# Kernel optimization log

Measured on AMD Instinct MI355X. Metric: run time of the kernel, lower is better.

Reference implementation:

```python
import jax, jax.numpy as jnp
import numpy as np

VOCAB = 100000
D = 128
B = 256
L = 2048  # leaves per tree (power of two -> complete binary tree)


def setup_inputs() -> dict:
    key = jax.random.key(0)
    k1, k2, k3, k4 = jax.random.split(key, 4)
    word_ids = jax.random.randint(k1, (B, L), 0, VOCAB)
    embedding = jax.random.normal(k2, (VOCAB, D), dtype=jnp.float32) * 0.1
    # torch nn.Linear(2*D, D): weight [D, 2*D], bias [D]
    W = jax.random.normal(k3, (D, 2 * D), dtype=jnp.float32) * (1.0 / np.sqrt(2 * D))
    b = jax.random.normal(k4, (D,), dtype=jnp.float32) * 0.01
    return {"word_ids": word_ids, "embedding": embedding, "W": W, "b": b}


def reference(word_ids, embedding, W, b):
    # Leaves: embedding lookup for every leaf of every tree. [B, L, D]
    x = embedding[word_ids]
    # Internal nodes, batched by depth: each level combines adjacent pairs
    # via linear(concat(left, right)). log2(L) levels (static unroll).
    while x.shape[1] > 1:
        left = x[:, 0::2, :]   # [B, n/2, D]
        right = x[:, 1::2, :]  # [B, n/2, D]
        pair = jnp.concatenate([left, right], axis=-1)  # [B, n/2, 2D]
        x = jnp.einsum('bnd,od->bno', pair, W) + b      # [B, n/2, D]
    return x[:, 0, :]  # root result per tree, [B, D]
```

## Files before the change

kernel.cpp:

```cpp
#include <hip/hip_runtime.h>


typedef __bf16 bf16x8 __attribute__((ext_vector_type(8)));
typedef __bf16 bf16x4 __attribute__((ext_vector_type(4)));
typedef float f32x4 __attribute__((ext_vector_type(4)));

#define STRIDE 136

__global__ void pack_w_kernel(const float* __restrict__ W,
                              __bf16* __restrict__ wpack) {
    const int f = blockIdx.x;
    const int tid = threadIdx.x;
    const int wv = tid >> 6, l = tid & 63;
    const int nl = f >> 3, kk = f & 7;
    const int o = ((wv << 1) + nl) * 16 + (l & 15);
    const int d = kk * 32 + ((l >> 4) << 3);
    const float* src = W + o * 256 + d;
    bf16x8 h;
#pragma unroll
    for (int j = 0; j < 8; ++j) h[j] = (__bf16)src[j];
    *(bf16x8*)(wpack + (size_t)(f * 256 + tid) * 8) = h;
}

template <int NOUT>
__device__ __forceinline__ void level_step(
    const __bf16* src0, const __bf16* src1, __bf16* dst,
    const bf16x8* wf, const float* bval, int wv, int q, int lm)
{
    const int ntm = (NOUT + 15) >> 4;
#pragma unroll
    for (int mt = 0; mt < ntm; ++mt) {
        const __bf16* src = mt ? src1 : src0;
        const int me = (NOUT >= 16) ? lm : (lm < NOUT ? lm : 0);
        f32x4 acc[2];
        acc[0] = f32x4{ bval[0], bval[0], bval[0], bval[0] };
        acc[1] = f32x4{ bval[1], bval[1], bval[1], bval[1] };
#pragma unroll
        for (int kh = 0; kh < 2; ++kh) {
            const int row = 2 * me + kh;
            bf16x8 af[4];
#pragma unroll
            for (int j = 0; j < 4; ++j)
                af[j] = *(const bf16x8*)&src[row * STRIDE + j * 32 + q * 8];
#pragma unroll
            for (int nl = 0; nl < 2; ++nl)
#pragma unroll
                for (int j = 0; j < 4; ++j)
                    acc[nl] = __builtin_amdgcn_mfma_f32_16x16x32_bf16(
                        af[j], wf[nl * 8 + kh * 4 + j], acc[nl], 0, 0, 0);
        }
#pragma unroll
        for (int nl = 0; nl < 2; ++nl) {
            const int col = (2 * wv + nl) * 16 + lm;
            const bf16x4 hv = __builtin_convertvector(acc[nl], bf16x4);
#pragma unroll
            for (int r = 0; r < 4; ++r) {
                const int row = mt * 16 + q * 4 + r;
                if (row < NOUT)
                    dst[row * STRIDE + col] = hv[r];
            }
        }
    }
    __syncthreads();
}

__device__ __forceinline__ void level_final(
    const __bf16* src, __bf16* yrow,
    const bf16x8* wf, const float* bval, int wv, int q, int lm)
{
    const int me = (lm < 2) ? lm : 0;
    f32x4 acc[2];
    acc[0] = f32x4{ bval[0], bval[0], bval[0], bval[0] };
    acc[1] = f32x4{ bval[1], bval[1], bval[1], bval[1] };
#pragma unroll
    for (int kh = 0; kh < 2; ++kh) {
        const int row = 2 * me + kh;
        bf16x8 af[4];
#pragma unroll
        for (int j = 0; j < 4; ++j)
            af[j] = *(const bf16x8*)&src[row * STRIDE + j * 32 + q * 8];
#pragma unroll
        for (int nl = 0; nl < 2; ++nl)
#pragma unroll
            for (int j = 0; j < 4; ++j)
                acc[nl] = __builtin_amdgcn_mfma_f32_16x16x32_bf16(
                    af[j], wf[nl * 8 + kh * 4 + j], acc[nl], 0, 0, 0);
    }
#pragma unroll
    for (int nl = 0; nl < 2; ++nl) {
        const int col = (2 * wv + nl) * 16 + lm;
        if (q == 0) {
            yrow[0 * 128 + col] = (__bf16)acc[nl][0];
            yrow[1 * 128 + col] = (__bf16)acc[nl][1];
        }
    }
}

__device__ __forceinline__ void gather64(
    const int* wb64, const float* emb, __bf16* dstA, int tid)
{
    int idreg[8];
#pragma unroll
    for (int i = 0; i < 8; ++i) idreg[i] = wb64[(tid >> 5) + 8 * i];
#pragma unroll
    for (int i = 0; i < 8; ++i) {
        const int row = (tid >> 5) + 8 * i;
        const int c4 = tid & 31;
        const f32x4 v = *(const f32x4*)(emb + (size_t)idreg[i] * 128 + c4 * 4);
        *(bf16x4*)&dstA[row * STRIDE + c4 * 4] =
            __builtin_convertvector(v, bf16x4);
    }
}

__global__ __launch_bounds__(256, 4) void tree128_kernel(
    const int* __restrict__ wid, const float* __restrict__ emb,
    const __bf16* __restrict__ wpack, const float* __restrict__ bias,
    __bf16* __restrict__ yout)
{
    __shared__ __align__(16) __bf16 bufA[64 * STRIDE];
    __shared__ __align__(16) __bf16 bufB[64 * STRIDE];
    const int tid = threadIdx.x;
    const int batch = blockIdx.x >> 4;
    const int grp = blockIdx.x & 15;
    const int wv = tid >> 6, ln = tid & 63, q = ln >> 4, lm = ln & 15;

    bf16x8 wf[16];
    const bf16x8* wp = (const bf16x8*)wpack;
#pragma unroll
    for (int f = 0; f < 16; ++f) wf[f] = wp[f * 256 + tid];
    float bval[2];
    bval[0] = bias[(2 * wv + 0) * 16 + lm];
    bval[1] = bias[(2 * wv + 1) * 16 + lm];

    const int* wb = wid + batch * 2048 + grp * 128;

    gather64(wb, emb, bufA, tid);
    __syncthreads();
    level_step<32>(bufA, bufA + 32 * STRIDE, bufB,
                   wf, bval, wv, q, lm);
    gather64(wb + 64, emb, bufA, tid);
    __syncthreads();
    level_step<32>(bufA, bufA + 32 * STRIDE, bufB + 32 * STRIDE,
                   wf, bval, wv, q, lm);
    level_step<32>(bufB, bufB + 32 * STRIDE, bufA, wf, bval, wv, q, lm);
    level_step<16>(bufA, nullptr,            bufB, wf, bval, wv, q, lm);
    level_step<8> (bufB, nullptr,            bufA, wf, bval, wv, q, lm);
    level_step<4> (bufA, nullptr,            bufB, wf, bval, wv, q, lm);
    level_final(bufB, yout + (size_t)(batch * 32 + grp * 2) * 128,
                wf, bval, wv, q, lm);
}

__global__ __launch_bounds__(256) void tree32_kernel(
    const __bf16* __restrict__ yin, const __bf16* __restrict__ wpack,
    const float* __restrict__ bias, float* __restrict__ out)
{
    __shared__ __align__(16) __bf16 buf0[32 * STRIDE];
    __shared__ __align__(16) __bf16 buf1[16 * STRIDE];
    const int tid = threadIdx.x;
    const int batch = blockIdx.x;
    const int wv = tid >> 6, ln = tid & 63, q = ln >> 4, lm = ln & 15;

    bf16x8 wf[16];
    const bf16x8* wp = (const bf16x8*)wpack;
#pragma unroll
    for (int f = 0; f < 16; ++f) wf[f] = wp[f * 256 + tid];
    float bval[2];
    bval[0] = bias[(2 * wv + 0) * 16 + lm];
    bval[1] = bias[(2 * wv + 1) * 16 + lm];

#pragma unroll
    for (int i = 0; i < 2; ++i) {
        const int flat = tid + 256 * i;
        const int row = flat >> 4;
        const int c8 = flat & 15;
        const bf16x8 v =
            *(const bf16x8*)(yin + (size_t)(batch * 32 + row) * 128 + c8 * 8);
        *(bf16x8*)&buf0[row * STRIDE + c8 * 8] = v;
    }
    __syncthreads();

    level_step<16>(buf0, nullptr, buf1, wf, bval, wv, q, lm);
    level_step<8> (buf1, nullptr, buf0, wf, bval, wv, q, lm);
    level_step<4> (buf0, nullptr, buf1, wf, bval, wv, q, lm);
    level_step<2> (buf1, nullptr, buf0, wf, bval, wv, q, lm);

    {
        f32x4 acc[2];
        acc[0] = f32x4{ bval[0], bval[0], bval[0], bval[0] };
        acc[1] = f32x4{ bval[1], bval[1], bval[1], bval[1] };
#pragma unroll
        for (int kh = 0; kh < 2; ++kh) {
            bf16x8 af[4];
#pragma unroll
            for (int j = 0; j < 4; ++j)
                af[j] = *(const bf16x8*)&buf0[kh * STRIDE + j * 32 + q * 8];
#pragma unroll
            for (int nl = 0; nl < 2; ++nl)
#pragma unroll
                for (int j = 0; j < 4; ++j)
                    acc[nl] = __builtin_amdgcn_mfma_f32_16x16x32_bf16(
                        af[j], wf[nl * 8 + kh * 4 + j], acc[nl], 0, 0, 0);
        }
#pragma unroll
        for (int nl = 0; nl < 2; ++nl) {
            const int col = (2 * wv + nl) * 16 + lm;
            if (q == 0) out[(size_t)batch * 128 + col] = acc[nl][0];
        }
    }
}

extern "C" void kernel_launch(void* const* d_in, const int* in_sizes, int n_in,
                              void* d_out, int out_size, void* d_ws, size_t ws_size,
                              hipStream_t stream) {
    const int*   wid = (const int*)d_in[0];
    const float* emb = (const float*)d_in[1];
    const float* W   = (const float*)d_in[2];
    const float* b   = (const float*)d_in[3];
    float* out = (float*)d_out;

    __bf16* wpack = (__bf16*)d_ws;
    __bf16* y     = wpack + 32768;

    pack_w_kernel<<<16, 256, 0, stream>>>(W, wpack);
    tree128_kernel<<<4096, 256, 0, stream>>>(wid, emb, wpack, b, y);
    tree32_kernel<<<256, 256, 0, stream>>>(y, wpack, b, out);
}
```

Measured before the change: 128.4 us.

## Software-pipeline embedding gathers with MFMA levels, two subtrees per block

Each block now processes two 128-leaf subtrees instead of one, and embedding gathers are split into an issue phase (global loads into registers) and a later write phase (convert and store to LDS). Loads for the next 64 leaves are issued before the current level's MFMA work, so gather latency overlaps compute. A third LDS buffer is added and occupancy is lowered from 4 to 3 blocks per CU, with half as many blocks launched. The extra register staging and LDS use reduce parallelism, which could offset the overlap gain.

```diff
diff --git a/kernel.cpp b/kernel.cpp
--- a/kernel.cpp
+++ b/kernel.cpp
@@ -96,32 +96,38 @@
     }
 }
 
-__device__ __forceinline__ void gather64(
-    const int* wb64, const float* emb, __bf16* dstA, int tid)
-{
-    int idreg[8];
-#pragma unroll
-    for (int i = 0; i < 8; ++i) idreg[i] = wb64[(tid >> 5) + 8 * i];
+__device__ __forceinline__ void gather_issue(
+    const int* wb64, const float* emb, int tid, f32x4 (&s)[8])
+{
+#pragma unroll
+    for (int i = 0; i < 8; ++i) {
+        const int id = wb64[(tid >> 5) + 8 * i];
+        s[i] = *(const f32x4*)(emb + (size_t)id * 128 + (tid & 31) * 4);
+    }
+}
+
+__device__ __forceinline__ void gather_write(
+    __bf16* dst, int tid, const f32x4 (&s)[8])
+{
 #pragma unroll
     for (int i = 0; i < 8; ++i) {
         const int row = (tid >> 5) + 8 * i;
-        const int c4 = tid & 31;
-        const f32x4 v = *(const f32x4*)(emb + (size_t)idreg[i] * 128 + c4 * 4);
-        *(bf16x4*)&dstA[row * STRIDE + c4 * 4] =
-            __builtin_convertvector(v, bf16x4);
-    }
-}
-
-__global__ __launch_bounds__(256, 4) void tree128_kernel(
+        *(bf16x4*)&dst[row * STRIDE + (tid & 31) * 4] =
+            __builtin_convertvector(s[i], bf16x4);
+    }
+}
+
+__global__ __launch_bounds__(256, 3) void tree128_kernel(
     const int* __restrict__ wid, const float* __restrict__ emb,
     const __bf16* __restrict__ wpack, const float* __restrict__ bias,
     __bf16* __restrict__ yout)
 {
     __shared__ __align__(16) __bf16 bufA[64 * STRIDE];
     __shared__ __align__(16) __bf16 bufB[64 * STRIDE];
+    __shared__ __align__(16) __bf16 bufC[64 * STRIDE];
     const int tid = threadIdx.x;
-    const int batch = blockIdx.x >> 4;
-    const int grp = blockIdx.x & 15;
+    const int batch = blockIdx.x >> 3;
+    const int pair = blockIdx.x & 7;
     const int wv = tid >> 6, ln = tid & 63, q = ln >> 4, lm = ln & 15;
 
     bf16x8 wf[16];
@@ -132,22 +138,34 @@
     bval[0] = bias[(2 * wv + 0) * 16 + lm];
     bval[1] = bias[(2 * wv + 1) * 16 + lm];
 
-    const int* wb = wid + batch * 2048 + grp * 128;
-
-    gather64(wb, emb, bufA, tid);
+    const int* wb = wid + batch * 2048 + pair * 256;
+    f32x4 st[8];
+
+    gather_issue(wb, emb, tid, st);
+    gather_write(bufC, tid, st);
     __syncthreads();
-    level_step<32>(bufA, bufA + 32 * STRIDE, bufB,
-                   wf, bval, wv, q, lm);
-    gather64(wb + 64, emb, bufA, tid);
-    __syncthreads();
-    level_step<32>(bufA, bufA + 32 * STRIDE, bufB + 32 * STRIDE,
-                   wf, bval, wv, q, lm);
-    level_step<32>(bufB, bufB + 32 * STRIDE, bufA, wf, bval, wv, q, lm);
-    level_step<16>(bufA, nullptr,            bufB, wf, bval, wv, q, lm);
-    level_step<8> (bufB, nullptr,            bufA, wf, bval, wv, q, lm);
-    level_step<4> (bufA, nullptr,            bufB, wf, bval, wv, q, lm);
-    level_final(bufB, yout + (size_t)(batch * 32 + grp * 2) * 128,
-                wf, bval, wv, q, lm);
+
+#pragma unroll
+    for (int g = 0; g < 2; ++g) {
+        const int* wg = wb + g * 128;
+        gather_issue(wg + 64, emb, tid, st);
+        level_step<32>(bufC, bufC + 32 * STRIDE, bufB, wf, bval, wv, q, lm);
+        gather_write(bufA, tid, st);
+        __syncthreads();
+        level_step<32>(bufA, bufA + 32 * STRIDE, bufB + 32 * STRIDE,
+                       wf, bval, wv, q, lm);
+        if (g == 0)
+            gather_issue(wb + 128, emb, tid, st);
+        level_step<32>(bufB, bufB + 32 * STRIDE, bufA, wf, bval, wv, q, lm);
+        if (g == 0)
+            gather_write(bufC, tid, st);
+        level_step<16>(bufA, nullptr, bufB, wf, bval, wv, q, lm);
+        level_step<8> (bufB, nullptr, bufA, wf, bval, wv, q, lm);
+        level_step<4> (bufA, nullptr, bufB, wf, bval, wv, q, lm);
+        level_final(bufB, yout + (size_t)(batch * 32 + (pair * 2 + g) * 2) * 128,
+                    wf, bval, wv, q, lm);
+        __syncthreads();
+    }
 }
 
 __global__ __launch_bounds__(256) void tree32_kernel(
@@ -222,6 +240,6 @@
     __bf16* y     = wpack + 32768;
 
     pack_w_kernel<<<16, 256, 0, stream>>>(W, wpack);
-    tree128_kernel<<<4096, 256, 0, stream>>>(wid, emb, wpack, b, y);
+    tree128_kernel<<<2048, 256, 0, stream>>>(wid, emb, wpack, b, y);
     tree32_kernel<<<256, 256, 0, stream>>>(y, wpack, b, out);
 }
```

New measurement: 128.6 us. No clear change (+0.1%).
